# Kernel tuning notes

Measured on AMD Instinct MI355X. Metric: run time of the kernel, lower is better.

## Reference

```python
import jax, jax.numpy as jnp
import numpy as np

B, N, DIM = 4, 2048, 512
HEADS, DK = 8, 64
SCALE = DK ** -0.5


def setup_inputs() -> dict:
    key = jax.random.key(0)
    k1, k2, k3, k4 = jax.random.split(key, 4)
    x = jax.random.normal(k1, (B, N, DIM), dtype=jnp.float32)
    # nn.Linear(dim, dim_key*heads, bias=False): y = x @ W.T; store W already transposed
    Wq = jax.random.normal(k2, (DIM, HEADS * DK), dtype=jnp.float32) * (DIM ** -0.5)
    Wk = jax.random.normal(k3, (DIM, HEADS * DK), dtype=jnp.float32) * (DIM ** -0.5)
    rel_content_bias = jax.random.normal(k4, (1, HEADS, 1, DK), dtype=jnp.float32)
    return {"x": x, "Wq": Wq, "Wk": Wk, "rel_content_bias": rel_content_bias}


def _split_heads(t, h):
    # [b, n, h*d] -> [b, h, n, d]
    b, n, hd = t.shape
    return t.reshape(b, n, h, hd // h).transpose(0, 2, 1, 3)


def reference(x, Wq, Wk, rel_content_bias):
    q = _split_heads(x @ Wq, HEADS) * SCALE          # [b, h, n, dk]
    k = _split_heads(x @ Wk, HEADS)                  # [b, h, n, dk]
    v = _split_heads(x, HEADS)                       # [b, h, n, dim/h]
    logits = jnp.einsum('bhid,bhjd->bhij', q + rel_content_bias, k)
    attn = jax.nn.sigmoid(logits)                    # no softmax normalization
    out = jnp.einsum('bhij,bhjd->bhid', attn, v)     # [b, h, n, dim/h]
    b, h, n, d = out.shape
    return out.transpose(0, 2, 1, 3).reshape(b, n, h * d)
```

## Files before the change

### kernel.cpp

```cpp
#include <hip/hip_runtime.h>
#include <hip/hip_bf16.h>
#include <stdint.h>

#define BB 4
#define NN 2048
#define DIMD 512
#define HH 8
#define DKK 64
#define MTOT (BB * NN)
constexpr float SCALE = 0.125f;

typedef __attribute__((ext_vector_type(4))) float f32x4;
typedef __attribute__((ext_vector_type(2))) float f32x2;
typedef __attribute__((ext_vector_type(8))) short bf16x8;
typedef __attribute__((ext_vector_type(4))) _Float16 f16x4;
typedef __attribute__((ext_vector_type(2))) __fp16 fp16v2;
typedef __attribute__((ext_vector_type(4))) __fp16 fp16v4;
typedef __attribute__((ext_vector_type(2))) unsigned int u32x2;

union pack8 { unsigned short s[8]; uint4 v; };
union fragu { u32x2 h[2]; bf16x8 v; };

__device__ __forceinline__ unsigned short f2bf(float f) {
  union { float f; uint32_t u; } v; v.f = f;
  uint32_t u = v.u;
  return (unsigned short)((u + 0x7FFFu + ((u >> 16) & 1u)) >> 16);
}

__device__ __forceinline__ unsigned short f2h(float f) {
  union { _Float16 h; unsigned short u; } c; c.h = (_Float16)f;
  return c.u;
}

__device__ __forceinline__ bf16x8 ld_frag(const unsigned short* p) {
  fragu f;
  f.h[0] = *(const u32x2*)p;
  f.h[1] = *(const u32x2*)(p + 4);
  return f.v;
}
__device__ __forceinline__ void st8(unsigned short* p, uint4 v) {
  *(u32x2*)p = (u32x2){v.x, v.y};
  *(u32x2*)(p + 4) = (u32x2){v.z, v.w};
}

__device__ __forceinline__ f16x4 sig_pack(f32x4 sv) {
  float e0 = __expf(-__builtin_fabsf(sv[0]));
  float e1 = __expf(-__builtin_fabsf(sv[1]));
  float e2 = __expf(-__builtin_fabsf(sv[2]));
  float e3 = __expf(-__builtin_fabsf(sv[3]));
  const f32x2 c3 = {-0.22184f, -0.22184f};
  const f32x2 c2 = {0.66550f, 0.66550f};
  const f32x2 c1 = {-0.94280f, -0.94280f};
  const f32x2 c0 = {0.49826f, 0.49826f};
  f32x2 eA = {e0, e1}, eB = {e2, e3};
  f32x2 pA = __builtin_elementwise_fma(
      __builtin_elementwise_fma(__builtin_elementwise_fma(c3, eA, c2), eA, c1),
      eA, c0);
  f32x2 pB = __builtin_elementwise_fma(
      __builtin_elementwise_fma(__builtin_elementwise_fma(c3, eB, c2), eB, c1),
      eB, c0);
  float r0 = __builtin_copysignf(pA.x, sv[0]);
  float r1 = __builtin_copysignf(pA.y, sv[1]);
  float r2 = __builtin_copysignf(pB.x, sv[2]);
  float r3 = __builtin_copysignf(pB.y, sv[3]);
  fp16v2 lo = __builtin_amdgcn_cvt_pkrtz(r0, r1);
  fp16v2 hi = __builtin_amdgcn_cvt_pkrtz(r2, r3);
  fp16v4 p;
  p.x = lo.x; p.y = lo.y; p.z = hi.x; p.w = hi.y;
  return __builtin_bit_cast(f16x4, p);
}

__global__ __launch_bounds__(256) void prep(const float* __restrict__ x,
                                            const float* __restrict__ wq,
                                            const float* __restrict__ wk,
                                            unsigned short* __restrict__ xb,
                                            unsigned short* __restrict__ xtf,
                                            unsigned short* __restrict__ wtq,
                                            unsigned short* __restrict__ wtk,
                                            float* __restrict__ vsum_p) {
  const int bx = blockIdx.x, tid = threadIdx.x;
  if (bx < 2048) {
    size_t base = ((size_t)bx * 256 + tid) * 8;
    float4 a = *(const float4*)(x + base);
    float4 b = *(const float4*)(x + base + 4);
    pack8 p;
    p.s[0] = f2bf(a.x); p.s[1] = f2bf(a.y); p.s[2] = f2bf(a.z); p.s[3] = f2bf(a.w);
    p.s[4] = f2bf(b.x); p.s[5] = f2bf(b.y); p.s[6] = f2bf(b.z); p.s[7] = f2bf(b.w);
    *(uint4*)(xb + base) = p.v;
  } else if (bx < 2304) {
    __shared__ float Pred[4][64];
    int q = bx - 2048;
    int b = q >> 6, r = q & 63;
    int dt = r >> 3, nt = r & 7;
    int dl = tid & 63, c = tid >> 6;
    int d = dt * 64 + dl;
    int n0 = nt * 256 + c * 64;
    const float* xp = x + ((size_t)b * NN + n0) * DIMD + d;
    unsigned short* dp = xtf + ((size_t)b * DIMD + d) * NN + n0;
    float s = 0.f;
#pragma unroll
    for (int g = 0; g < 8; g++) {
      pack8 pa;
#pragma unroll
      for (int k = 0; k < 8; k++) {
        float v = xp[(size_t)(g * 8 + k) * DIMD];
        s += v;
        pa.s[k] = f2h(v);
      }
      *(uint4*)(dp + g * 8) = pa.v;
    }
    Pred[c][dl] = s;
    __syncthreads();
    if (c == 0) {
      float t = Pred[0][dl] + Pred[1][dl] + Pred[2][dl] + Pred[3][dl];
      vsum_p[((size_t)b * 8 + nt) * DIMD + d] = t;
    }
  } else {
    __shared__ __align__(16) unsigned short T[64][68];
    int q = bx - 2304;
    const float* w = (q >= 64) ? wk : wq;
    unsigned short* wt = (q >= 64) ? wtk : wtq;
    int r = q & 63;
    int kt = r >> 3, nt = r & 7;
    const int k0 = kt * 64, n0 = nt * 64;
#pragma unroll
    for (int rr = 0; rr < 16; rr++) {
      int idx = tid + rr * 256;
      int kl = idx >> 6, nl = idx & 63;
      T[nl][kl] = f2bf(w[(size_t)(k0 + kl) * DIMD + n0 + nl]);
    }
    __syncthreads();
#pragma unroll
    for (int rr = 0; rr < 2; rr++) {
      int idx = tid + rr * 256;
      int nl = idx >> 3, c = idx & 7;
      fragu f;
      f.h[0] = *(const u32x2*)&T[nl][c * 8];
      f.h[1] = *(const u32x2*)&T[nl][c * 8 + 4];
      uint4 v;
      v.x = f.h[0].x; v.y = f.h[0].y; v.z = f.h[1].x; v.w = f.h[1].y;
      *(uint4*)(wt + (size_t)(n0 + nl) * DIMD + k0 + c * 8) = v;
    }
  }
}

__global__ __launch_bounds__(512, 4) void qk_gemm(const unsigned short* __restrict__ xb,
                                                  const unsigned short* __restrict__ wtq,
                                                  const unsigned short* __restrict__ wtk,
                                                  const float* __restrict__ bias,
                                                  unsigned short* __restrict__ qout,
                                                  unsigned short* __restrict__ kout) {
  __shared__ __align__(16) unsigned short Als[128][68];
  __shared__ __align__(16) unsigned short Bls[128][68];
  const int mb = blockIdx.x, nb = blockIdx.y;
  const bool isQ = (nb < 4);
  const unsigned short* wt = isQ ? wtq : wtk;
  unsigned short* outp = isQ ? qout : kout;
  const int n0 = (nb & 3) * 128, m0 = mb * 128;
  const int tid = threadIdx.x;
  const int wave = tid >> 6, lane = tid & 63;
  const int quad = lane >> 4, l16 = lane & 15;
  const int wm = wave >> 2, wn = wave & 3;

  f32x4 acc[4][2];
#pragma unroll
  for (int a = 0; a < 4; a++)
#pragma unroll
    for (int c = 0; c < 2; c++) acc[a][c] = (f32x4){0.f, 0.f, 0.f, 0.f};

  const int srow[2] = {tid >> 3, (tid + 512) >> 3};
  const int scol = (tid & 7) * 8;
  uint4 pa[2], pb[2];
#pragma unroll
  for (int r = 0; r < 2; r++) {
    pa[r] = *(const uint4*)(xb + (size_t)(m0 + srow[r]) * DIMD + scol);
    pb[r] = *(const uint4*)(wt + (size_t)(n0 + srow[r]) * DIMD + scol);
  }

  for (int k0 = 0; k0 < DIMD; k0 += 64) {
    __syncthreads();
#pragma unroll
    for (int r = 0; r < 2; r++) {
      st8(&Als[srow[r]][scol], pa[r]);
      st8(&Bls[srow[r]][scol], pb[r]);
    }
    __syncthreads();
    if (k0 + 64 < DIMD) {
#pragma unroll
      for (int r = 0; r < 2; r++) {
        pa[r] = *(const uint4*)(xb + (size_t)(m0 + srow[r]) * DIMD + k0 + 64 + scol);
        pb[r] = *(const uint4*)(wt + (size_t)(n0 + srow[r]) * DIMD + k0 + 64 + scol);
      }
    }
#pragma unroll
    for (int ks = 0; ks < 2; ks++) {
      bf16x8 af[4], bfr[2];
#pragma unroll
      for (int t = 0; t < 4; t++)
        af[t] = ld_frag(&Als[wm * 64 + t * 16 + l16][quad * 8 + ks * 32]);
#pragma unroll
      for (int t = 0; t < 2; t++)
        bfr[t] = ld_frag(&Bls[wn * 32 + t * 16 + l16][quad * 8 + ks * 32]);
#pragma unroll
      for (int tm = 0; tm < 4; tm++)
#pragma unroll
        for (int tn = 0; tn < 2; tn++)
          acc[tm][tn] =
              __builtin_amdgcn_mfma_f32_16x16x32_bf16(af[tm], bfr[tn], acc[tm][tn], 0, 0, 0);
    }
  }
#pragma unroll
  for (int tm = 0; tm < 4; tm++) {
#pragma unroll
    for (int tn = 0; tn < 2; tn++) {
#pragma unroll
      for (int r = 0; r < 4; r++) {
        int row = m0 + wm * 64 + tm * 16 + quad * 4 + r;
        int gcol = n0 + wn * 32 + tn * 16 + l16;
        float v = acc[tm][tn][r];
        if (isQ) v = v * SCALE + bias[gcol];
        outp[(size_t)row * DIMD + gcol] = f2bf(v);
      }
    }
  }
}

__global__ __launch_bounds__(512, 4) void attn(const unsigned short* __restrict__ qb,
                                               const unsigned short* __restrict__ kb,
                                               const unsigned short* __restrict__ xtf,
                                               const float* __restrict__ vsum_p,
                                               float* __restrict__ out) {
  __shared__ __align__(16) char smem[69632];
  unsigned short* Kall = (unsigned short*)smem;
  unsigned short* Vall = Kall + 4 * 4352;
  float* R0 = (float*)smem;

  const int bh = blockIdx.x, it = blockIdx.y;
  const int b = bh >> 3, h = bh & 7;
  const int i0 = it * 128;
  const int tid = threadIdx.x;
  const int lane = tid & 63;
  const int grp = tid >> 8;
  const int wv = (tid >> 6) & 3;
  const int gtid = tid & 255;
  const int quad = lane >> 4, l16 = lane & 15;

  bf16x8 qf[2][2];
  int irow[2];
#pragma unroll
  for (int s_ = 0; s_ < 2; s_++) {
    irow[s_] = i0 + wv * 32 + s_ * 16 + l16;
    const unsigned short* qp = qb + ((size_t)b * NN + irow[s_]) * DIMD + h * DKK + quad * 8;
    qf[s_][0] = *(const bf16x8*)qp;
    qf[s_][1] = *(const bf16x8*)(qp + 32);
  }

  f32x4 o[2][4];
#pragma unroll
  for (int s_ = 0; s_ < 2; s_++)
#pragma unroll
    for (int td = 0; td < 4; td++) o[s_][td] = (f32x4){0.f, 0.f, 0.f, 0.f};

  const unsigned short* kbase = kb + (size_t)b * NN * DIMD + h * DKK;
  const unsigned short* vbase = xtf + ((size_t)b * DIMD + h * DKK) * NN;
  unsigned short* Kg0 = Kall + (grp * 2 + 0) * 4352;
  unsigned short* Kg1 = Kall + (grp * 2 + 1) * 4352;
  unsigned short* Vg0 = Vall + (grp * 2 + 0) * 4352;
  unsigned short* Vg1 = Vall + (grp * 2 + 1) * 4352;
  const int jbase = grp * 1024;

  const int trow[2] = {gtid >> 3, (gtid + 256) >> 3};
  const int tcol = (gtid & 7) * 8;
  uint4 pk[2], pv[2];

  auto prefetch = [&](int t) {
    const int j0 = jbase + t * 64;
#pragma unroll
    for (int r = 0; r < 2; r++) {
      pk[r] = *(const uint4*)(kbase + (size_t)(j0 + trow[r]) * DIMD + tcol);
      pv[r] = *(const uint4*)(vbase + (size_t)trow[r] * NN + j0 + tcol);
    }
  };
  auto stage = [&](unsigned short* Kg, unsigned short* Vg) {
#pragma unroll
    for (int r = 0; r < 2; r++) {
      st8(&Kg[trow[r] * 68 + tcol], pk[r]);
      st8(&Vg[trow[r] * 68 + tcol], pv[r]);
    }
  };
  auto compute = [&](const unsigned short* Kg, const unsigned short* Vg) {
    __builtin_amdgcn_s_setprio(1);
#pragma unroll
    for (int t = 0; t < 4; t++) {
      bf16x8 kf0 = ld_frag(&Kg[(t * 16 + l16) * 68 + quad * 8]);
      bf16x8 kf1 = ld_frag(&Kg[(t * 16 + l16) * 68 + quad * 8 + 32]);
      f16x4 pf[2];
#pragma unroll
      for (int s_ = 0; s_ < 2; s_++) {
        f32x4 sv = (f32x4){0.f, 0.f, 0.f, 0.f};
        sv = __builtin_amdgcn_mfma_f32_16x16x32_bf16(kf0, qf[s_][0], sv, 0, 0, 0);
        sv = __builtin_amdgcn_mfma_f32_16x16x32_bf16(kf1, qf[s_][1], sv, 0, 0, 0);
        pf[s_] = sig_pack(sv);
      }
#pragma unroll
      for (int td = 0; td < 4; td++) {
        f16x4 vf = __builtin_bit_cast(
            f16x4, *(const u32x2*)&Vg[(td * 16 + l16) * 68 + t * 16 + quad * 4]);
        o[0][td] = __builtin_amdgcn_mfma_f32_16x16x16f16(vf, pf[0], o[0][td], 0, 0, 0);
        o[1][td] = __builtin_amdgcn_mfma_f32_16x16x16f16(vf, pf[1], o[1][td], 0, 0, 0);
      }
    }
    __builtin_amdgcn_s_setprio(0);
  };

  prefetch(0);
  stage(Kg0, Vg0);
  prefetch(1);
  __syncthreads();

  for (int itr = 0; itr < 16; itr += 2) {
    stage(Kg1, Vg1);
    if (itr + 2 < 16) prefetch(itr + 2);
    compute(Kg0, Vg0);
    __syncthreads();
    if (itr + 2 < 16) {
      stage(Kg0, Vg0);
      if (itr + 3 < 16) prefetch(itr + 3);
    }
    compute(Kg1, Vg1);
    __syncthreads();
  }

  if (grp == 1) {
#pragma unroll
    for (int s_ = 0; s_ < 2; s_++)
#pragma unroll
      for (int td = 0; td < 4; td++) {
        int base = (wv * 32 + s_ * 16 + l16) * 66 + td * 16 + quad * 4;
        *(f32x2*)&R0[base] = (f32x2){o[s_][td][0], o[s_][td][1]};
        *(f32x2*)&R0[base + 2] = (f32x2){o[s_][td][2], o[s_][td][3]};
      }
  }
  __syncthreads();
  if (grp == 0) {
    const float* vp = vsum_p + (size_t)b * 8 * DIMD + h * DKK;
    f32x4 vs[4];
#pragma unroll
    for (int td = 0; td < 4; td++) {
      f32x4 a = (f32x4){0.f, 0.f, 0.f, 0.f};
#pragma unroll
      for (int p = 0; p < 8; p++) {
        f32x4 t = *(const f32x4*)&vp[(size_t)p * DIMD + td * 16 + quad * 4];
        a[0] += t[0]; a[1] += t[1]; a[2] += t[2]; a[3] += t[3];
      }
      vs[td] = a;
    }
#pragma unroll
    for (int s_ = 0; s_ < 2; s_++) {
#pragma unroll
      for (int td = 0; td < 4; td++) {
        int base = (wv * 32 + s_ * 16 + l16) * 66 + td * 16 + quad * 4;
        f32x2 a = *(const f32x2*)&R0[base];
        f32x2 c = *(const f32x2*)&R0[base + 2];
        o[s_][td][0] += a.x + 0.5f * vs[td][0];
        o[s_][td][1] += a.y + 0.5f * vs[td][1];
        o[s_][td][2] += c.x + 0.5f * vs[td][2];
        o[s_][td][3] += c.y + 0.5f * vs[td][3];
        float* op = out + ((size_t)b * NN + irow[s_]) * DIMD + h * DKK + td * 16 + quad * 4;
        *(f32x4*)op = o[s_][td];
      }
    }
  }
}

extern "C" void kernel_launch(void* const* d_in, const int* in_sizes, int n_in,
                              void* d_out, int out_size, void* d_ws, size_t ws_size,
                              hipStream_t stream) {
  const float* x = (const float*)d_in[0];
  const float* Wq = (const float*)d_in[1];
  const float* Wk = (const float*)d_in[2];
  const float* bias = (const float*)d_in[3];
  float* out = (float*)d_out;

  unsigned short* ws = (unsigned short*)d_ws;
  unsigned short* xb = ws;
  unsigned short* xtf = xb + (size_t)MTOT * DIMD;
  unsigned short* wtq = xtf + (size_t)MTOT * DIMD;
  unsigned short* wtk = wtq + (size_t)DIMD * DIMD;
  unsigned short* qb = wtk + (size_t)DIMD * DIMD;
  unsigned short* kb = qb + (size_t)MTOT * DIMD;
  float* vsum_p = (float*)(kb + (size_t)MTOT * DIMD);

  prep<<<dim3(2432), 256, 0, stream>>>(x, Wq, Wk, xb, xtf, wtq, wtk, vsum_p);
  qk_gemm<<<dim3(64, 8), 512, 0, stream>>>(xb, wtq, wtk, bias, qb, kb);
  attn<<<dim3(32, 16), 512, 0, stream>>>(qb, kb, xtf, vsum_p, out);
}
```

Before: 155.9 us.

## Fuse x bf16 conversion into QK GEMM, use exp2 sigmoid, single-buffer attention LDS

Removes the separate x-to-bf16 pass from the prep kernel. The QK GEMM now loads fp32 x and converts it to bf16 while loading, which drops one full write and read of an intermediate bf16 copy of x. The log2(e) factor is folded into the Q scale and bias so the sigmoid can use the hardware exp2 directly. The attention kernel changes from double-buffered to single-buffered LDS with a register prefetch, halving shared memory to allow more occupancy, at the cost of an extra barrier per iteration and less load/compute overlap.

```diff
diff --git a/kernel.cpp b/kernel.cpp
--- a/kernel.cpp
+++ b/kernel.cpp
@@ -9,6 +9,7 @@
 #define DKK 64
 #define MTOT (BB * NN)
 constexpr float SCALE = 0.125f;
+constexpr float L2E = 1.44269504089f;
 
 typedef __attribute__((ext_vector_type(4))) float f32x4;
 typedef __attribute__((ext_vector_type(2))) float f32x2;
@@ -44,10 +45,10 @@
 }
 
 __device__ __forceinline__ f16x4 sig_pack(f32x4 sv) {
-  float e0 = __expf(-__builtin_fabsf(sv[0]));
-  float e1 = __expf(-__builtin_fabsf(sv[1]));
-  float e2 = __expf(-__builtin_fabsf(sv[2]));
-  float e3 = __expf(-__builtin_fabsf(sv[3]));
+  float e0 = __builtin_amdgcn_exp2f(-__builtin_fabsf(sv[0]));
+  float e1 = __builtin_amdgcn_exp2f(-__builtin_fabsf(sv[1]));
+  float e2 = __builtin_amdgcn_exp2f(-__builtin_fabsf(sv[2]));
+  float e3 = __builtin_amdgcn_exp2f(-__builtin_fabsf(sv[3]));
   const f32x2 c3 = {-0.22184f, -0.22184f};
   const f32x2 c2 = {0.66550f, 0.66550f};
   const f32x2 c1 = {-0.94280f, -0.94280f};
@@ -73,23 +74,14 @@
 __global__ __launch_bounds__(256) void prep(const float* __restrict__ x,
                                             const float* __restrict__ wq,
                                             const float* __restrict__ wk,
-                                            unsigned short* __restrict__ xb,
                                             unsigned short* __restrict__ xtf,
                                             unsigned short* __restrict__ wtq,
                                             unsigned short* __restrict__ wtk,
                                             float* __restrict__ vsum_p) {
   const int bx = blockIdx.x, tid = threadIdx.x;
-  if (bx < 2048) {
-    size_t base = ((size_t)bx * 256 + tid) * 8;
-    float4 a = *(const float4*)(x + base);
-    float4 b = *(const float4*)(x + base + 4);
-    pack8 p;
-    p.s[0] = f2bf(a.x); p.s[1] = f2bf(a.y); p.s[2] = f2bf(a.z); p.s[3] = f2bf(a.w);
-    p.s[4] = f2bf(b.x); p.s[5] = f2bf(b.y); p.s[6] = f2bf(b.z); p.s[7] = f2bf(b.w);
-    *(uint4*)(xb + base) = p.v;
-  } else if (bx < 2304) {
+  if (bx < 256) {
     __shared__ float Pred[4][64];
-    int q = bx - 2048;
+    int q = bx;
     int b = q >> 6, r = q & 63;
     int dt = r >> 3, nt = r & 7;
     int dl = tid & 63, c = tid >> 6;
@@ -117,7 +109,7 @@
     }
   } else {
     __shared__ __align__(16) unsigned short T[64][68];
-    int q = bx - 2304;
+    int q = bx - 256;
     const float* w = (q >= 64) ? wk : wq;
     unsigned short* wt = (q >= 64) ? wtk : wtq;
     int r = q & 63;
@@ -144,7 +136,7 @@
   }
 }
 
-__global__ __launch_bounds__(512, 4) void qk_gemm(const unsigned short* __restrict__ xb,
+__global__ __launch_bounds__(512, 4) void qk_gemm(const float* __restrict__ x,
                                                   const unsigned short* __restrict__ wtq,
                                                   const unsigned short* __restrict__ wtk,
                                                   const float* __restrict__ bias,
@@ -171,9 +163,20 @@
   const int srow[2] = {tid >> 3, (tid + 512) >> 3};
   const int scol = (tid & 7) * 8;
   uint4 pa[2], pb[2];
+
+  auto loadA = [&](int r, int k0) -> uint4 {
+    const float* ap = x + (size_t)(m0 + srow[r]) * DIMD + k0 + scol;
+    float4 a = *(const float4*)ap;
+    float4 b = *(const float4*)(ap + 4);
+    pack8 p;
+    p.s[0] = f2bf(a.x); p.s[1] = f2bf(a.y); p.s[2] = f2bf(a.z); p.s[3] = f2bf(a.w);
+    p.s[4] = f2bf(b.x); p.s[5] = f2bf(b.y); p.s[6] = f2bf(b.z); p.s[7] = f2bf(b.w);
+    return p.v;
+  };
+
 #pragma unroll
   for (int r = 0; r < 2; r++) {
-    pa[r] = *(const uint4*)(xb + (size_t)(m0 + srow[r]) * DIMD + scol);
+    pa[r] = loadA(r, 0);
     pb[r] = *(const uint4*)(wt + (size_t)(n0 + srow[r]) * DIMD + scol);
   }
 
@@ -188,7 +191,7 @@
     if (k0 + 64 < DIMD) {
 #pragma unroll
       for (int r = 0; r < 2; r++) {
-        pa[r] = *(const uint4*)(xb + (size_t)(m0 + srow[r]) * DIMD + k0 + 64 + scol);
+        pa[r] = loadA(r, k0 + 64);
         pb[r] = *(const uint4*)(wt + (size_t)(n0 + srow[r]) * DIMD + k0 + 64 + scol);
       }
     }
@@ -213,12 +216,13 @@
   for (int tm = 0; tm < 4; tm++) {
 #pragma unroll
     for (int tn = 0; tn < 2; tn++) {
+      int gcol = n0 + wn * 32 + tn * 16 + l16;
+      float bl = isQ ? bias[gcol] * L2E : 0.f;
 #pragma unroll
       for (int r = 0; r < 4; r++) {
         int row = m0 + wm * 64 + tm * 16 + quad * 4 + r;
-        int gcol = n0 + wn * 32 + tn * 16 + l16;
         float v = acc[tm][tn][r];
-        if (isQ) v = v * SCALE + bias[gcol];
+        if (isQ) v = v * (SCALE * L2E) + bl;
         outp[(size_t)row * DIMD + gcol] = f2bf(v);
       }
     }
@@ -230,9 +234,9 @@
                                                const unsigned short* __restrict__ xtf,
                                                const float* __restrict__ vsum_p,
                                                float* __restrict__ out) {
-  __shared__ __align__(16) char smem[69632];
+  __shared__ __align__(16) char smem[34816];
   unsigned short* Kall = (unsigned short*)smem;
-  unsigned short* Vall = Kall + 4 * 4352;
+  unsigned short* Vall = Kall + 2 * 64 * 68;
   float* R0 = (float*)smem;
 
   const int bh = blockIdx.x, it = blockIdx.y;
@@ -263,32 +267,36 @@
 
   const unsigned short* kbase = kb + (size_t)b * NN * DIMD + h * DKK;
   const unsigned short* vbase = xtf + ((size_t)b * DIMD + h * DKK) * NN;
-  unsigned short* Kg0 = Kall + (grp * 2 + 0) * 4352;
-  unsigned short* Kg1 = Kall + (grp * 2 + 1) * 4352;
-  unsigned short* Vg0 = Vall + (grp * 2 + 0) * 4352;
-  unsigned short* Vg1 = Vall + (grp * 2 + 1) * 4352;
+  unsigned short* Kg = Kall + grp * (64 * 68);
+  unsigned short* Vg = Vall + grp * (64 * 68);
   const int jbase = grp * 1024;
 
   const int trow[2] = {gtid >> 3, (gtid + 256) >> 3};
   const int tcol = (gtid & 7) * 8;
   uint4 pk[2], pv[2];
-
-  auto prefetch = [&](int t) {
-    const int j0 = jbase + t * 64;
-#pragma unroll
-    for (int r = 0; r < 2; r++) {
-      pk[r] = *(const uint4*)(kbase + (size_t)(j0 + trow[r]) * DIMD + tcol);
-      pv[r] = *(const uint4*)(vbase + (size_t)trow[r] * NN + j0 + tcol);
-    }
-  };
-  auto stage = [&](unsigned short* Kg, unsigned short* Vg) {
+#pragma unroll
+  for (int r = 0; r < 2; r++) {
+    pk[r] = *(const uint4*)(kbase + (size_t)(jbase + trow[r]) * DIMD + tcol);
+    pv[r] = *(const uint4*)(vbase + (size_t)trow[r] * NN + jbase + tcol);
+  }
+
+  for (int itr = 0; itr < 16; itr++) {
+    __syncthreads();
 #pragma unroll
     for (int r = 0; r < 2; r++) {
       st8(&Kg[trow[r] * 68 + tcol], pk[r]);
       st8(&Vg[trow[r] * 68 + tcol], pv[r]);
     }
-  };
-  auto compute = [&](const unsigned short* Kg, const unsigned short* Vg) {
+    __syncthreads();
+    if (itr < 15) {
+      const int j0 = jbase + (itr + 1) * 64;
+#pragma unroll
+      for (int r = 0; r < 2; r++) {
+        pk[r] = *(const uint4*)(kbase + (size_t)(j0 + trow[r]) * DIMD + tcol);
+        pv[r] = *(const uint4*)(vbase + (size_t)trow[r] * NN + j0 + tcol);
+      }
+    }
+
     __builtin_amdgcn_s_setprio(1);
 #pragma unroll
     for (int t = 0; t < 4; t++) {
@@ -311,26 +319,9 @@
       }
     }
     __builtin_amdgcn_s_setprio(0);
-  };
-
-  prefetch(0);
-  stage(Kg0, Vg0);
-  prefetch(1);
+  }
+
   __syncthreads();
-
-  for (int itr = 0; itr < 16; itr += 2) {
-    stage(Kg1, Vg1);
-    if (itr + 2 < 16) prefetch(itr + 2);
-    compute(Kg0, Vg0);
-    __syncthreads();
-    if (itr + 2 < 16) {
-      stage(Kg0, Vg0);
-      if (itr + 3 < 16) prefetch(itr + 3);
-    }
-    compute(Kg1, Vg1);
-    __syncthreads();
-  }
-
   if (grp == 1) {
 #pragma unroll
     for (int s_ = 0; s_ < 2; s_++)
@@ -383,15 +374,14 @@
   float* out = (float*)d_out;
 
   unsigned short* ws = (unsigned short*)d_ws;
-  unsigned short* xb = ws;
-  unsigned short* xtf = xb + (size_t)MTOT * DIMD;
+  unsigned short* xtf = ws;
   unsigned short* wtq = xtf + (size_t)MTOT * DIMD;
   unsigned short* wtk = wtq + (size_t)DIMD * DIMD;
   unsigned short* qb = wtk + (size_t)DIMD * DIMD;
   unsigned short* kb = qb + (size_t)MTOT * DIMD;
   float* vsum_p = (float*)(kb + (size_t)MTOT * DIMD);
 
-  prep<<<dim3(2432), 256, 0, stream>>>(x, Wq, Wk, xb, xtf, wtq, wtk, vsum_p);
-  qk_gemm<<<dim3(64, 8), 512, 0, stream>>>(xb, wtq, wtk, bias, qb, kb);
+  prep<<<dim3(384), 256, 0, stream>>>(x, Wq, Wk, xtf, wtq, wtk, vsum_p);
+  qk_gemm<<<dim3(64, 8), 512, 0, stream>>>(x, wtq, wtk, bias, qb, kb);
   attn<<<dim3(32, 16), 512, 0, stream>>>(qb, kb, xtf, vsum_p, out);
 }
```

New measurement: 150.3 us. 3.6% less time.
